# Kernel optimization log

Hardware: AMD Instinct MI355X
Metric: run time of the kernel (lower is better)

The kernel has to match this reference:

```python
import jax, jax.numpy as jnp
import numpy as np

# dims (match init_kwargs)
B, S, HID = 2, 2048, 2048
NH = 16
DN = 128   # qk_nope_head_dim
DR = 64    # qk_rope_head_dim
DV = 128   # v_head_dim
QLR = 1536 # q_lora_rank
KVLR = 512 # kv_lora_rank
QHD = DN + DR  # 192
ROPE_BASE = 10000.0
EPS = 1e-6


def rms_norm(x, w):
    # ZeroCenteredRMSNorm: weight is zero-centered, scale = (1 + w)
    var = jnp.mean(x * x, axis=-1, keepdims=True)
    return x * jax.lax.rsqrt(var + EPS) * (1.0 + w)


def rotate_half(x):
    d = x.shape[-1] // 2
    return jnp.concatenate([-x[..., d:], x[..., :d]], axis=-1)


def deinterleave(x):
    # rearrange '(d_pairs two) -> (two d_pairs)'
    return jnp.concatenate([x[..., 0::2], x[..., 1::2]], axis=-1)


def setup_inputs() -> dict:
    key = jax.random.key(0)
    ks = jax.random.split(key, 8)
    s = 0.02
    return {
        "hidden_states": jax.random.normal(ks[0], (B, S, HID), jnp.float32),
        "position_ids": jnp.arange(S, dtype=jnp.int32),
        "Wq_down": jax.random.normal(ks[1], (HID, QLR), jnp.float32) * s,
        "q_norm_w": jnp.zeros((QLR,), jnp.float32),
        "Wq_up": jax.random.normal(ks[2], (QLR, NH * QHD), jnp.float32) * s,
        "Wkv_down": jax.random.normal(ks[3], (HID, KVLR + DR), jnp.float32) * s,
        "kv_norm_w": jnp.zeros((KVLR,), jnp.float32),
        "Wkv_up": jax.random.normal(ks[4], (KVLR, NH * (DN + DV)), jnp.float32) * s,
        "W_gate": jax.random.normal(ks[5], (HID, NH * DV), jnp.float32) * s,
        "W_out": jax.random.normal(ks[6], (NH * DV, HID), jnp.float32) * s,
    }


def reference(hidden_states, position_ids, Wq_down, q_norm_w, Wq_up,
              Wkv_down, kv_norm_w, Wkv_up, W_gate, W_out):
    bsz, q_len, _ = hidden_states.shape
    pos = jnp.broadcast_to(position_ids[None, :], (bsz, q_len))  # [b,s]

    # Q path: down-proj -> RMSNorm -> up-proj -> [b,h,s,QHD]
    q = rms_norm(hidden_states @ Wq_down, q_norm_w) @ Wq_up
    q = q.reshape(bsz, q_len, NH, QHD).transpose(0, 2, 1, 3)
    q_nope, q_rope = q[..., :DN], q[..., DN:]

    # KV path: joint down-proj -> split latent / rope key
    ckv = hidden_states @ Wkv_down                     # [b,s,KVLR+DR]
    c_kv, k_rope = ckv[..., :KVLR], ckv[..., KVLR:]
    k_rope = k_rope[:, None, :, :]                     # [b,1,s,DR]
    kv = rms_norm(c_kv, kv_norm_w) @ Wkv_up            # [b,s,NH*(DN+DV)]
    kv = kv.reshape(bsz, q_len, NH, DN + DV).transpose(0, 2, 1, 3)
    k_nope, v = kv[..., :DN], kv[..., DN:]

    # partial RoPE on rope dims (with the '(pairs two)->(two pairs)' permute)
    inv_freq = 1.0 / (ROPE_BASE ** (jnp.arange(0, DR, 2, dtype=jnp.float32) / DR))
    freqs = pos[..., None].astype(jnp.float32) * inv_freq  # [b,s,DR/2]
    emb = jnp.concatenate([freqs, freqs], axis=-1)          # [b,s,DR]
    cos = jnp.cos(emb)[:, None, :, :]                       # [b,1,s,DR]
    sin = jnp.sin(emb)[:, None, :, :]
    q_r = deinterleave(q_rope)
    k_r = deinterleave(k_rope)
    q_r = q_r * cos + rotate_half(q_r) * sin
    k_r = k_r * cos + rotate_half(k_r) * sin

    query = jnp.concatenate([q_nope, q_r], axis=-1)                       # [b,h,s,QHD]
    key = jnp.concatenate([k_nope, jnp.broadcast_to(k_r, k_nope.shape[:-1] + (DR,))], axis=-1)

    scores = jnp.einsum('bhqd,bhkd->bhqk', query, key) / np.sqrt(QHD)
    attn = jax.nn.softmax(scores, axis=-1)
    out = jnp.einsum('bhqk,bhkd->bhqd', attn, v)                          # [b,h,s,DV]
    out = out.transpose(0, 2, 1, 3)                                       # [b,s,h,DV]

    gate = jax.nn.sigmoid(hidden_states @ W_gate).reshape(bsz, q_len, NH, DV)
    out = (out * gate).reshape(bsz, q_len, NH * DV)
    return out @ W_out
```

## Files before the change

kernel.cpp:

```cpp
#include <hip/hip_runtime.h>
#include <math.h>

#define BT 2
#define SL 2048
#define HIDN 2048
#define NHEADS 16
#define DNOPE 128
#define DROPE 64
#define DVAL 128
#define QHEAD 192
#define QLRANK 1536
#define KVLRANK 512
#define TTOK (BT * SL)
#define FN 4224
#define FC_CKV 1536
#define FC_ROPE 2048
#define FC_GATE 2176

typedef unsigned short u16;
typedef u16 u16x4 __attribute__((ext_vector_type(4)));
typedef u16 u16x8 __attribute__((ext_vector_type(8)));
typedef short bf16x8 __attribute__((ext_vector_type(8)));
typedef float f32x4 __attribute__((ext_vector_type(4)));

__device__ __forceinline__ u16 f2b(float f) {
    union { float f; unsigned u; } v; v.f = f;
    unsigned r = v.u + 0x7FFFu + ((v.u >> 16) & 1u);
    return (u16)(r >> 16);
}
__device__ __forceinline__ float b2f(u16 h) {
    union { unsigned u; float f; } v; v.u = ((unsigned)h) << 16;
    return v.f;
}
__device__ __forceinline__ float fexp2(float x) {
    float r;
    asm("v_exp_f32 %0, %1" : "=v"(r) : "v"(x));
    return r;
}

__device__ __forceinline__ void gl2lds16(const u16* g, u16* l) {
    __builtin_amdgcn_global_load_lds((const __attribute__((address_space(1))) unsigned int*)g,
                                     (__attribute__((address_space(3))) unsigned int*)l, 16, 0, 0);
}

__device__ __forceinline__ void tcast_tile(const float* __restrict__ in, u16* __restrict__ out,
                                           int R, int C, int tx, int ty, int t) {
    __shared__ u16 tile[64][72];
    const int c0 = tx * 64, r0 = ty * 64;
    const int tr = t >> 4, tc4 = (t & 15) * 4;
#pragma unroll
    for (int i = 0; i < 4; ++i) {
        const int r = tr + i * 16;
        const float4 v = *(const float4*)&in[(size_t)(r0 + r) * C + c0 + tc4];
        u16x4 u;
        u.x = f2b(v.x); u.y = f2b(v.y); u.z = f2b(v.z); u.w = f2b(v.w);
        *(u16x4*)&tile[r][tc4] = u;
    }
    __syncthreads();
#pragma unroll
    for (int i = 0; i < 4; ++i) {
        const int rr = tr + i * 16;
        u16x4 u;
        u.x = tile[tc4 + 0][rr];
        u.y = tile[tc4 + 1][rr];
        u.z = tile[tc4 + 2][rr];
        u.w = tile[tc4 + 3][rr];
        *(u16x4*)&out[(size_t)(c0 + rr) * R + r0 + tc4] = u;
    }
}

__global__ __launch_bounds__(256) void precast_k(
    const float* __restrict__ Wq_down, const float* __restrict__ Wq_up,
    const float* __restrict__ Wkv_down, const float* __restrict__ Wkv_up,
    const float* __restrict__ W_gate, const float* __restrict__ W_out,
    const float* __restrict__ hs, u16* __restrict__ wqd_t, u16* __restrict__ wqu_t,
    u16* __restrict__ wkvd_t, u16* __restrict__ wkvu_t, u16* __restrict__ wg_t,
    u16* __restrict__ wo_t, u16* __restrict__ hs16) {
    const int tid = blockIdx.x;
    const int t = threadIdx.x;
    if (tid >= 4768) {
        int i = (tid - 4768) * 256 + t;
        for (; i < TTOK * HIDN / 4; i += 2048 * 256) {
            const float4 v = ((const float4*)hs)[i];
            u16x4 u;
            u.x = f2b(v.x); u.y = f2b(v.y); u.z = f2b(v.z); u.w = f2b(v.w);
            ((u16x4*)hs16)[i] = u;
        }
        return;
    }
    if (tid < 768) {
        tcast_tile(Wq_down, wqd_t, 2048, 1536, tid % 24, tid / 24, t);
    } else if (tid < 1920) {
        const int i = tid - 768;
        tcast_tile(Wq_up, wqu_t, 1536, 3072, i % 48, i / 48, t);
    } else if (tid < 2208) {
        const int i = tid - 1920;
        tcast_tile(Wkv_down, wkvd_t, 2048, 576, i % 9, i / 9, t);
    } else if (tid < 2720) {
        const int i = tid - 2208;
        tcast_tile(Wkv_up, wkvu_t, 512, 4096, i % 64, i / 64, t);
    } else if (tid < 3744) {
        const int i = tid - 2720;
        tcast_tile(W_gate, wg_t, 2048, 2048, i % 32, i / 32, t);
    } else {
        const int i = tid - 3744;
        tcast_tile(W_out, wo_t, 2048, 2048, i % 32, i / 32, t);
    }
}

template <int MODE>
__global__ __launch_bounds__(256) void gemm_bf16_k(const u16* __restrict__ A,
                                                   const u16* __restrict__ Bt,
                                                   void* __restrict__ Cv, u16* __restrict__ C2,
                                                   int M, int N, int K) {
    __shared__ u16 As[128 * 64];
    __shared__ u16 Bs[128 * 64];
    const int t = threadIdx.x;
    const int nx = gridDim.x;
    const int bid = blockIdx.x + nx * blockIdx.y;
    const int cpx = (nx * gridDim.y) >> 3;
    const int swz = (bid & 7) * cpx + (bid >> 3);
    const int bn = (swz % nx) * 128, bm = (swz / nx) * 128;
    const int w = t >> 6, lane = t & 63;
    const int wr = (w >> 1) * 64, wc = (w & 1) * 64;
    const int lr = lane & 15, lg = lane >> 4;

    const int srow = w * 32 + (lane >> 3);
    const int scol = ((lane & 7) ^ ((lane >> 3) & 7)) * 8;
    const u16* Ag = A + (size_t)(bm + srow) * K + scol;
    const u16* Bg = Bt + (size_t)(bn + srow) * K + scol;
    u16* Asl = As + w * 2048;
    u16* Bsl = Bs + w * 2048;

    f32x4 acc[4][4];
#pragma unroll
    for (int i = 0; i < 4; ++i)
#pragma unroll
        for (int j = 0; j < 4; ++j) acc[i][j] = 0.f;

    for (int k0 = 0; k0 < K; k0 += 64) {
        __syncthreads();
#pragma unroll
        for (int j = 0; j < 4; ++j) gl2lds16(Ag + (size_t)(j * 8) * K + k0, Asl + j * 512);
#pragma unroll
        for (int j = 0; j < 4; ++j) gl2lds16(Bg + (size_t)(j * 8) * K + k0, Bsl + j * 512);
        __syncthreads();
#pragma unroll
        for (int kk = 0; kk < 2; ++kk) {
            bf16x8 af[4], bfr[4];
#pragma unroll
            for (int mi = 0; mi < 4; ++mi) {
                const int row = wr + mi * 16 + lr;
                const int idx = (row * 64 + kk * 32 + lg * 8) ^ ((row & 7) << 3);
                af[mi] = *(const bf16x8*)&As[idx];
            }
#pragma unroll
            for (int ni = 0; ni < 4; ++ni) {
                const int row = wc + ni * 16 + lr;
                const int idx = (row * 64 + kk * 32 + lg * 8) ^ ((row & 7) << 3);
                bfr[ni] = *(const bf16x8*)&Bs[idx];
            }
#pragma unroll
            for (int mi = 0; mi < 4; ++mi)
#pragma unroll
                for (int ni = 0; ni < 4; ++ni)
                    acc[mi][ni] = __builtin_amdgcn_mfma_f32_16x16x32_bf16(af[mi], bfr[ni],
                                                                          acc[mi][ni], 0, 0, 0);
        }
    }
#pragma unroll
    for (int mi = 0; mi < 4; ++mi)
#pragma unroll
        for (int ni = 0; ni < 4; ++ni) {
            const int row0 = bm + wr + mi * 16 + lg * 4;
            const int col = bn + wc + ni * 16 + lr;
            if (MODE == 3) {
                const int h = col >> 8, cd = col & 255;
                if (cd < 128) {
#pragma unroll
                    for (int r = 0; r < 4; ++r)
                        ((u16*)Cv)[(size_t)(row0 + r) * 2048 + h * 128 + cd] =
                            f2b(acc[mi][ni][r]);
                } else {
                    u16x4 pk;
                    pk.x = f2b(acc[mi][ni][0]);
                    pk.y = f2b(acc[mi][ni][1]);
                    pk.z = f2b(acc[mi][ni][2]);
                    pk.w = f2b(acc[mi][ni][3]);
                    const int bb = row0 >> 11;
                    *(u16x4*)&C2[((size_t)((bb * 16 + h) * 128 + (cd - 128))) * SL +
                                 (row0 & (SL - 1))] = pk;
                }
            } else {
#pragma unroll
                for (int r = 0; r < 4; ++r) {
                    float v = acc[mi][ni][r];
                    if (MODE == 2 && col >= FC_GATE) v = 1.f / (1.f + __expf(-v));
                    if (MODE == 1)
                        ((float*)Cv)[(size_t)(row0 + r) * N + col] = v;
                    else
                        ((u16*)Cv)[(size_t)(row0 + r) * N + col] = f2b(v);
                }
            }
        }
}

__global__ __launch_bounds__(256) void rms2_k(const u16* __restrict__ fout,
                                              const float* __restrict__ qw,
                                              const float* __restrict__ kw, u16* __restrict__ qn,
                                              u16* __restrict__ kvn) {
    const int rid = blockIdx.x;
    const bool isq = rid < TTOK;
    const int row = isq ? rid : rid - TTOK;
    const int n = isq ? QLRANK : KVLRANK;
    const u16* x = fout + (size_t)row * FN + (isq ? 0 : FC_CKV);
    const float* w = isq ? qw : kw;
    u16* y = isq ? (qn + (size_t)row * QLRANK) : (kvn + (size_t)row * KVLRANK);
    const int t = threadIdx.x;
    float ss = 0.f;
    for (int d = t * 4; d < n; d += 1024) {
        const u16x4 u = *(const u16x4*)&x[d];
        const float a = b2f(u.x), b = b2f(u.y), c = b2f(u.z), e = b2f(u.w);
        ss += a * a + b * b + c * c + e * e;
    }
    ss += __shfl_down(ss, 32);
    ss += __shfl_down(ss, 16);
    ss += __shfl_down(ss, 8);
    ss += __shfl_down(ss, 4);
    ss += __shfl_down(ss, 2);
    ss += __shfl_down(ss, 1);
    __shared__ float red[5];
    if ((t & 63) == 0) red[t >> 6] = ss;
    __syncthreads();
    if (t == 0) red[4] = rsqrtf((red[0] + red[1] + red[2] + red[3]) / (float)n + 1e-6f);
    __syncthreads();
    const float sc = red[4];
    for (int d = t * 4; d < n; d += 1024) {
        const u16x4 u = *(const u16x4*)&x[d];
        const float4 wv = *(const float4*)&w[d];
        u16x4 o;
        o.x = f2b(b2f(u.x) * sc * (1.f + wv.x));
        o.y = f2b(b2f(u.y) * sc * (1.f + wv.y));
        o.z = f2b(b2f(u.z) * sc * (1.f + wv.z));
        o.w = f2b(b2f(u.w) * sc * (1.f + wv.w));
        *(u16x4*)&y[d] = o;
    }
}

__global__ __launch_bounds__(64) void rope_k(u16* __restrict__ q, const u16* __restrict__ fout,
                                             u16* __restrict__ kr, const int* __restrict__ pos_ids) {
    const int tok = blockIdx.x * 2 + (threadIdx.x >> 5);
    const int j = threadIdx.x & 31;
    const int s = tok & (SL - 1);
    const float pos = (float)pos_ids[s];
    const float inv = 1.f / powf(10000.f, (float)(2 * j) / 64.f);
    const float f = pos * inv;
    const float c = cosf(f), sn = sinf(f);
    const u16* kc = fout + (size_t)tok * FN + FC_ROPE;
    const unsigned kp = *(const unsigned*)&kc[2 * j];
    const float ke = b2f((u16)(kp & 0xffff)), ko = b2f((u16)(kp >> 16));
    kr[tok * 64 + j] = f2b(ke * c - ko * sn);
    kr[tok * 64 + 32 + j] = f2b(ko * c + ke * sn);
#pragma unroll
    for (int h = 0; h < NHEADS; ++h) {
        u16* qb = q + (size_t)tok * (NHEADS * QHEAD) + h * QHEAD + DNOPE;
        const unsigned qp = *(const unsigned*)&qb[2 * j];
        const float qe = b2f((u16)(qp & 0xffff)), qo = b2f((u16)(qp >> 16));
        qb[j] = f2b(qe * c - qo * sn);
        qb[32 + j] = f2b(qo * c + qe * sn);
    }
}

#define PSTR 76
__global__ __launch_bounds__(256, 2) void mla_attn_k(const u16* __restrict__ qbuf,
                                                     const u16* __restrict__ knope,
                                                     const u16* __restrict__ kr,
                                                     const u16* __restrict__ vT,
                                                     const u16* __restrict__ gateb,
                                                     u16* __restrict__ outg) {
    __shared__ u16 Ks[64 * 200];
    __shared__ u16 Vt[128 * 72];
    __shared__ u16 Ps[4 * 32 * PSTR];
    const int bh = blockIdx.x;
    const int b = bh >> 4, h = bh & 15;
    const int q0 = blockIdx.y * 128;
    const int t = threadIdx.x, w = t >> 6, lane = t & 63;
    const int lr = lane & 15, lg = lane >> 4;
    const float qs = 0.07216878364870322f * 1.4426950408889634f;
    const float THR = 8.f * 1.4426950408889634f;

    int kRow[6], kC8[6];
#pragma unroll
    for (int c = 0; c < 6; ++c) {
        const int i = t + c * 256;
        kRow[c] = i / 24;
        kC8[c] = (i % 24) * 8;
    }
    int vRow[4], vC8[4];
#pragma unroll
    for (int c = 0; c < 4; ++c) {
        const int i = t + c * 256;
        vRow[c] = i >> 3;
        vC8[c] = (i & 7) * 8;
    }

    bf16x8 aq[2][6];
#pragma unroll
    for (int mi = 0; mi < 2; ++mi) {
        const int qrow = b * SL + q0 + w * 32 + mi * 16 + lr;
#pragma unroll
        for (int ks = 0; ks < 6; ++ks) {
            const u16x8 raw = *(const u16x8*)&qbuf[(size_t)qrow * (NHEADS * QHEAD) + h * QHEAD +
                                                   ks * 32 + lg * 8];
            bf16x8 o;
#pragma unroll
            for (int j = 0; j < 8; ++j) o[j] = (short)f2b(b2f(raw[j]) * qs);
            aq[mi][ks] = o;
        }
    }
    bf16x8 ones;
#pragma unroll
    for (int j = 0; j < 8; ++j) ones[j] = (short)0x3F80;

    f32x4 O[2][8];
#pragma unroll
    for (int mi = 0; mi < 2; ++mi)
#pragma unroll
        for (int df = 0; df < 8; ++df) O[mi][df] = 0.f;
    f32x4 Ol[2];
    Ol[0] = 0.f;
    Ol[1] = 0.f;
    float m[2][4];
#pragma unroll
    for (int mi = 0; mi < 2; ++mi)
#pragma unroll
        for (int r = 0; r < 4; ++r) m[mi][r] = -INFINITY;

    u16x8 kreg[6], vreg[4];
#define ATTN_ISSUE_K(K0)                                                                     \
    {                                                                                        \
        _Pragma("unroll") for (int c = 0; c < 6; ++c) {                                      \
            const int tok = b * SL + (K0) + kRow[c];                                         \
            kreg[c] = (kC8[c] < 128)                                                         \
                          ? *(const u16x8*)&knope[(size_t)tok * 2048 + h * 128 + kC8[c]]     \
                          : *(const u16x8*)&kr[(size_t)tok * 64 + (kC8[c] - 128)];           \
        }                                                                                    \
    }
#define ATTN_ISSUE_V(K0)                                                                     \
    {                                                                                        \
        _Pragma("unroll") for (int c = 0; c < 4; ++c)                                        \
            vreg[c] = *(const u16x8*)&vT[(size_t)(bh * 128 + vRow[c]) * SL + (K0) + vC8[c]]; \
    }

    ATTN_ISSUE_K(0);
    ATTN_ISSUE_V(0);

    for (int it = 0; it < SL / 64; ++it) {
        __syncthreads();
#pragma unroll
        for (int c = 0; c < 6; ++c) *(u16x8*)&Ks[kRow[c] * 200 + kC8[c]] = kreg[c];
#pragma unroll
        for (int c = 0; c < 4; ++c) *(u16x8*)&Vt[vRow[c] * 72 + vC8[c]] = vreg[c];
        __syncthreads();
        const bool more = (it + 1) < SL / 64;
        const int kn = (it + 1) * 64;
        if (more) ATTN_ISSUE_K(kn);

        f32x4 s[2][4];
#pragma unroll
        for (int mi = 0; mi < 2; ++mi)
#pragma unroll
            for (int nf = 0; nf < 4; ++nf) s[mi][nf] = 0.f;
#pragma unroll
        for (int ks = 0; ks < 6; ++ks) {
#pragma unroll
            for (int nf = 0; nf < 4; ++nf) {
                const bf16x8 bk = *(const bf16x8*)&Ks[(nf * 16 + lr) * 200 + ks * 32 + lg * 8];
                s[0][nf] = __builtin_amdgcn_mfma_f32_16x16x32_bf16(aq[0][ks], bk, s[0][nf], 0, 0, 0);
                s[1][nf] = __builtin_amdgcn_mfma_f32_16x16x32_bf16(aq[1][ks], bk, s[1][nf], 0, 0, 0);
            }
        }

        float g = -INFINITY;
#pragma unroll
        for (int mi = 0; mi < 2; ++mi)
#pragma unroll
            for (int r = 0; r < 4; ++r) {
                const float lmax =
                    fmaxf(fmaxf(s[mi][0][r], s[mi][1][r]), fmaxf(s[mi][2][r], s[mi][3][r]));
                g = fmaxf(g, lmax - m[mi][r]);
            }
        g = fmaxf(g, __shfl_xor(g, 1));
        g = fmaxf(g, __shfl_xor(g, 2));
        g = fmaxf(g, __shfl_xor(g, 4));
        g = fmaxf(g, __shfl_xor(g, 8));
        g = fmaxf(g, __shfl_xor(g, 16));
        g = fmaxf(g, __shfl_xor(g, 32));
        if (!(g <= THR)) {
#pragma unroll
            for (int mi = 0; mi < 2; ++mi)
#pragma unroll
                for (int r = 0; r < 4; ++r) {
                    float lm =
                        fmaxf(fmaxf(s[mi][0][r], s[mi][1][r]), fmaxf(s[mi][2][r], s[mi][3][r]));
                    lm = fmaxf(lm, __shfl_xor(lm, 1));
                    lm = fmaxf(lm, __shfl_xor(lm, 2));
                    lm = fmaxf(lm, __shfl_xor(lm, 4));
                    lm = fmaxf(lm, __shfl_xor(lm, 8));
                    const float mn = fmaxf(m[mi][r], lm);
                    const float al = fexp2(m[mi][r] - mn);
                    m[mi][r] = mn;
                    Ol[mi][r] *= al;
#pragma unroll
                    for (int df = 0; df < 8; ++df) O[mi][df][r] *= al;
                }
        }

#pragma unroll
        for (int mi = 0; mi < 2; ++mi) {
            const int pb = w * 32 * PSTR + mi * 16 * PSTR;
#pragma unroll
            for (int r = 0; r < 4; ++r) {
                const float mn = m[mi][r];
                const int prow = pb + (lg * 4 + r) * PSTR + lr;
                Ps[prow] = f2b(fexp2(s[mi][0][r] - mn));
                Ps[prow + 16] = f2b(fexp2(s[mi][1][r] - mn));
                Ps[prow + 32] = f2b(fexp2(s[mi][2][r] - mn));
                Ps[prow + 48] = f2b(fexp2(s[mi][3][r] - mn));
            }
        }

        if (more) ATTN_ISSUE_V(kn);

        bf16x8 pa[2][2];
#pragma unroll
        for (int mi = 0; mi < 2; ++mi)
#pragma unroll
            for (int ks2 = 0; ks2 < 2; ++ks2)
                pa[mi][ks2] =
                    *(const bf16x8*)&Ps[w * 32 * PSTR + (mi * 16 + lr) * PSTR + ks2 * 32 + lg * 8];
#pragma unroll
        for (int mi = 0; mi < 2; ++mi)
#pragma unroll
            for (int ks2 = 0; ks2 < 2; ++ks2)
                Ol[mi] = __builtin_amdgcn_mfma_f32_16x16x32_bf16(pa[mi][ks2], ones, Ol[mi], 0, 0, 0);
#pragma unroll
        for (int df = 0; df < 8; ++df)
#pragma unroll
            for (int ks2 = 0; ks2 < 2; ++ks2) {
                const bf16x8 bv = *(const bf16x8*)&Vt[(df * 16 + lr) * 72 + ks2 * 32 + lg * 8];
                O[0][df] = __builtin_amdgcn_mfma_f32_16x16x32_bf16(pa[0][ks2], bv, O[0][df], 0, 0, 0);
                O[1][df] = __builtin_amdgcn_mfma_f32_16x16x32_bf16(pa[1][ks2], bv, O[1][df], 0, 0, 0);
            }
    }
#pragma unroll
    for (int mi = 0; mi < 2; ++mi) {
        float invl[4];
#pragma unroll
        for (int r = 0; r < 4; ++r) invl[r] = 1.f / Ol[mi][r];
#pragma unroll
        for (int df = 0; df < 8; ++df)
#pragma unroll
            for (int r = 0; r < 4; ++r) {
                const int qq = b * SL + q0 + w * 32 + mi * 16 + lg * 4 + r;
                const int col = h * DVAL + df * 16 + lr;
                const float o = O[mi][df][r] * invl[r];
                const float gg = b2f(gateb[(size_t)qq * FN + col]);
                outg[(size_t)qq * (NHEADS * DVAL) + col] = f2b(o * gg);
            }
    }
}

extern "C" void kernel_launch(void* const* d_in, const int* in_sizes, int n_in, void* d_out,
                              int out_size, void* d_ws, size_t ws_size, hipStream_t stream) {
    const float* hs = (const float*)d_in[0];
    const int* pos = (const int*)d_in[1];
    const float* Wq_down = (const float*)d_in[2];
    const float* q_norm_w = (const float*)d_in[3];
    const float* Wq_up = (const float*)d_in[4];
    const float* Wkv_down = (const float*)d_in[5];
    const float* kv_norm_w = (const float*)d_in[6];
    const float* Wkv_up = (const float*)d_in[7];
    const float* W_gate = (const float*)d_in[8];
    const float* W_out = (const float*)d_in[9];
    float* out = (float*)d_out;

    u16* p = (u16*)d_ws;
    u16* hs16 = p;      p += (size_t)TTOK * HIDN;
    u16* wdown_t = p;   p += (size_t)FN * HIDN;
    u16* wqd_t = wdown_t;
    u16* wkvd_t = wdown_t + (size_t)QLRANK * HIDN;
    u16* wg_t = wdown_t + (size_t)FC_GATE * HIDN;
    u16* wqu_t = p;     p += (size_t)(NHEADS * QHEAD) * QLRANK;
    u16* wkvu_t = p;    p += (size_t)(NHEADS * 256) * KVLRANK;
    u16* wo_t = p;      p += (size_t)HIDN * (NHEADS * DVAL);
    u16* fout = p;      p += (size_t)TTOK * FN;
    u16* qdownN = p;    p += (size_t)TTOK * QLRANK;
    u16* qbuf = p;      p += (size_t)TTOK * (NHEADS * QHEAD);
    u16* kvn = p;       p += (size_t)TTOK * KVLRANK;
    u16* knope = p;     p += (size_t)TTOK * (NHEADS * DNOPE);
    u16* krb = p;       p += (size_t)TTOK * DROPE;
    u16* vTg = p;       p += (size_t)32 * 128 * SL;
    u16* outg = p;      p += (size_t)TTOK * (NHEADS * DVAL);

    const dim3 blk(256);

    precast_k<<<dim3(6816), blk, 0, stream>>>(Wq_down, Wq_up, Wkv_down, Wkv_up, W_gate, W_out, hs,
                                              wqd_t, wqu_t, wkvd_t, wkvu_t, wg_t, wo_t, hs16);

    gemm_bf16_k<2><<<dim3(FN / 128, TTOK / 128), blk, 0, stream>>>(hs16, wdown_t, fout, nullptr,
                                                                   TTOK, FN, HIDN);
    rms2_k<<<dim3(2 * TTOK), blk, 0, stream>>>(fout, q_norm_w, kv_norm_w, qdownN, kvn);
    gemm_bf16_k<0><<<dim3((NHEADS * QHEAD) / 128, TTOK / 128), blk, 0, stream>>>(
        qdownN, wqu_t, qbuf, nullptr, TTOK, NHEADS * QHEAD, QLRANK);
    gemm_bf16_k<3><<<dim3((NHEADS * 256) / 128, TTOK / 128), blk, 0, stream>>>(
        kvn, wkvu_t, knope, vTg, TTOK, NHEADS * 256, KVLRANK);
    rope_k<<<dim3(TTOK / 2), dim3(64), 0, stream>>>(qbuf, fout, krb, pos);

    mla_attn_k<<<dim3(32, SL / 128), blk, 0, stream>>>(qbuf, knope, krb, vTg, fout + FC_GATE, outg);

    gemm_bf16_k<1><<<dim3(HIDN / 128, TTOK / 128), blk, 0, stream>>>(outg, wo_t, out, nullptr, TTOK,
                                                                     HIDN, NHEADS * DVAL);
}
```

Baseline: 440.4 us.

## Merge Q and KV up-projection GEMMs into one launch; add MFMA wave priority in attention

```diff
diff --git a/kernel.cpp b/kernel.cpp
--- a/kernel.cpp
+++ b/kernel.cpp
@@ -111,8 +111,7 @@
 template <int MODE>
 __global__ __launch_bounds__(256) void gemm_bf16_k(const u16* __restrict__ A,
                                                    const u16* __restrict__ Bt,
-                                                   void* __restrict__ Cv, u16* __restrict__ C2,
-                                                   int M, int N, int K) {
+                                                   void* __restrict__ Cv, int M, int N, int K) {
     __shared__ u16 As[128 * 64];
     __shared__ u16 Bs[128 * 64];
     const int t = threadIdx.x;
@@ -174,13 +173,101 @@
         for (int ni = 0; ni < 4; ++ni) {
             const int row0 = bm + wr + mi * 16 + lg * 4;
             const int col = bn + wc + ni * 16 + lr;
-            if (MODE == 3) {
+#pragma unroll
+            for (int r = 0; r < 4; ++r) {
+                float v = acc[mi][ni][r];
+                if (MODE == 2 && col >= FC_GATE) v = 1.f / (1.f + __expf(-v));
+                if (MODE == 1)
+                    ((float*)Cv)[(size_t)(row0 + r) * N + col] = v;
+                else
+                    ((u16*)Cv)[(size_t)(row0 + r) * N + col] = f2b(v);
+            }
+        }
+}
+
+__global__ __launch_bounds__(256) void gemm_up_k(const u16* __restrict__ Aq,
+                                                 const u16* __restrict__ Akv,
+                                                 const u16* __restrict__ Btq,
+                                                 const u16* __restrict__ Btkv,
+                                                 u16* __restrict__ qbuf, u16* __restrict__ knope,
+                                                 u16* __restrict__ vT) {
+    __shared__ u16 As[128 * 64];
+    __shared__ u16 Bs[128 * 64];
+    const int t = threadIdx.x;
+    const int nx = gridDim.x;
+    const int bid = blockIdx.x + nx * blockIdx.y;
+    const int cpx = (nx * gridDim.y) >> 3;
+    const int swz = (bid & 7) * cpx + (bid >> 3);
+    const int tn = swz % nx, bm = (swz / nx) * 128;
+    const bool isq = tn < 24;
+    const int K = isq ? QLRANK : KVLRANK;
+    const int bn = (isq ? tn : tn - 24) * 128;
+    const u16* A = isq ? Aq : Akv;
+    const u16* Bt = isq ? Btq : Btkv;
+
+    const int w = t >> 6, lane = t & 63;
+    const int wr = (w >> 1) * 64, wc = (w & 1) * 64;
+    const int lr = lane & 15, lg = lane >> 4;
+
+    const int srow = w * 32 + (lane >> 3);
+    const int scol = ((lane & 7) ^ ((lane >> 3) & 7)) * 8;
+    const u16* Ag = A + (size_t)(bm + srow) * K + scol;
+    const u16* Bg = Bt + (size_t)(bn + srow) * K + scol;
+    u16* Asl = As + w * 2048;
+    u16* Bsl = Bs + w * 2048;
+
+    f32x4 acc[4][4];
+#pragma unroll
+    for (int i = 0; i < 4; ++i)
+#pragma unroll
+        for (int j = 0; j < 4; ++j) acc[i][j] = 0.f;
+
+    for (int k0 = 0; k0 < K; k0 += 64) {
+        __syncthreads();
+#pragma unroll
+        for (int j = 0; j < 4; ++j) gl2lds16(Ag + (size_t)(j * 8) * K + k0, Asl + j * 512);
+#pragma unroll
+        for (int j = 0; j < 4; ++j) gl2lds16(Bg + (size_t)(j * 8) * K + k0, Bsl + j * 512);
+        __syncthreads();
+#pragma unroll
+        for (int kk = 0; kk < 2; ++kk) {
+            bf16x8 af[4], bfr[4];
+#pragma unroll
+            for (int mi = 0; mi < 4; ++mi) {
+                const int row = wr + mi * 16 + lr;
+                const int idx = (row * 64 + kk * 32 + lg * 8) ^ ((row & 7) << 3);
+                af[mi] = *(const bf16x8*)&As[idx];
+            }
+#pragma unroll
+            for (int ni = 0; ni < 4; ++ni) {
+                const int row = wc + ni * 16 + lr;
+                const int idx = (row * 64 + kk * 32 + lg * 8) ^ ((row & 7) << 3);
+                bfr[ni] = *(const bf16x8*)&Bs[idx];
+            }
+#pragma unroll
+            for (int mi = 0; mi < 4; ++mi)
+#pragma unroll
+                for (int ni = 0; ni < 4; ++ni)
+                    acc[mi][ni] = __builtin_amdgcn_mfma_f32_16x16x32_bf16(af[mi], bfr[ni],
+                                                                          acc[mi][ni], 0, 0, 0);
+        }
+    }
+#pragma unroll
+    for (int mi = 0; mi < 4; ++mi)
+#pragma unroll
+        for (int ni = 0; ni < 4; ++ni) {
+            const int row0 = bm + wr + mi * 16 + lg * 4;
+            const int col = bn + wc + ni * 16 + lr;
+            if (isq) {
+#pragma unroll
+                for (int r = 0; r < 4; ++r)
+                    qbuf[(size_t)(row0 + r) * (NHEADS * QHEAD) + col] = f2b(acc[mi][ni][r]);
+            } else {
                 const int h = col >> 8, cd = col & 255;
                 if (cd < 128) {
 #pragma unroll
                     for (int r = 0; r < 4; ++r)
-                        ((u16*)Cv)[(size_t)(row0 + r) * 2048 + h * 128 + cd] =
-                            f2b(acc[mi][ni][r]);
+                        knope[(size_t)(row0 + r) * 2048 + h * 128 + cd] = f2b(acc[mi][ni][r]);
                 } else {
                     u16x4 pk;
                     pk.x = f2b(acc[mi][ni][0]);
@@ -188,18 +275,8 @@
                     pk.z = f2b(acc[mi][ni][2]);
                     pk.w = f2b(acc[mi][ni][3]);
                     const int bb = row0 >> 11;
-                    *(u16x4*)&C2[((size_t)((bb * 16 + h) * 128 + (cd - 128))) * SL +
+                    *(u16x4*)&vT[((size_t)((bb * 16 + h) * 128 + (cd - 128))) * SL +
                                  (row0 & (SL - 1))] = pk;
-                }
-            } else {
-#pragma unroll
-                for (int r = 0; r < 4; ++r) {
-                    float v = acc[mi][ni][r];
-                    if (MODE == 2 && col >= FC_GATE) v = 1.f / (1.f + __expf(-v));
-                    if (MODE == 1)
-                        ((float*)Cv)[(size_t)(row0 + r) * N + col] = v;
-                    else
-                        ((u16*)Cv)[(size_t)(row0 + r) * N + col] = f2b(v);
                 }
             }
         }
@@ -371,6 +448,7 @@
         for (int mi = 0; mi < 2; ++mi)
 #pragma unroll
             for (int nf = 0; nf < 4; ++nf) s[mi][nf] = 0.f;
+        __builtin_amdgcn_s_setprio(1);
 #pragma unroll
         for (int ks = 0; ks < 6; ++ks) {
 #pragma unroll
@@ -380,6 +458,7 @@
                 s[1][nf] = __builtin_amdgcn_mfma_f32_16x16x32_bf16(aq[1][ks], bk, s[1][nf], 0, 0, 0);
             }
         }
+        __builtin_amdgcn_s_setprio(0);
 
         float g = -INFINITY;
 #pragma unroll
@@ -439,6 +518,7 @@
             for (int ks2 = 0; ks2 < 2; ++ks2)
                 pa[mi][ks2] =
                     *(const bf16x8*)&Ps[w * 32 * PSTR + (mi * 16 + lr) * PSTR + ks2 * 32 + lg * 8];
+        __builtin_amdgcn_s_setprio(1);
 #pragma unroll
         for (int mi = 0; mi < 2; ++mi)
 #pragma unroll
@@ -452,6 +532,7 @@
                 O[0][df] = __builtin_amdgcn_mfma_f32_16x16x32_bf16(pa[0][ks2], bv, O[0][df], 0, 0, 0);
                 O[1][df] = __builtin_amdgcn_mfma_f32_16x16x32_bf16(pa[1][ks2], bv, O[1][df], 0, 0, 0);
             }
+        __builtin_amdgcn_s_setprio(0);
     }
 #pragma unroll
     for (int mi = 0; mi < 2; ++mi) {
@@ -508,17 +589,15 @@
     precast_k<<<dim3(6816), blk, 0, stream>>>(Wq_down, Wq_up, Wkv_down, Wkv_up, W_gate, W_out, hs,
                                               wqd_t, wqu_t, wkvd_t, wkvu_t, wg_t, wo_t, hs16);
 
-    gemm_bf16_k<2><<<dim3(FN / 128, TTOK / 128), blk, 0, stream>>>(hs16, wdown_t, fout, nullptr,
-                                                                   TTOK, FN, HIDN);
+    gemm_bf16_k<2><<<dim3(FN / 128, TTOK / 128), blk, 0, stream>>>(hs16, wdown_t, fout, TTOK, FN,
+                                                                   HIDN);
     rms2_k<<<dim3(2 * TTOK), blk, 0, stream>>>(fout, q_norm_w, kv_norm_w, qdownN, kvn);
-    gemm_bf16_k<0><<<dim3((NHEADS * QHEAD) / 128, TTOK / 128), blk, 0, stream>>>(
-        qdownN, wqu_t, qbuf, nullptr, TTOK, NHEADS * QHEAD, QLRANK);
-    gemm_bf16_k<3><<<dim3((NHEADS * 256) / 128, TTOK / 128), blk, 0, stream>>>(
-        kvn, wkvu_t, knope, vTg, TTOK, NHEADS * 256, KVLRANK);
+    gemm_up_k<<<dim3(56, TTOK / 128), blk, 0, stream>>>(qdownN, kvn, wqu_t, wkvu_t, qbuf, knope,
+                                                        vTg);
     rope_k<<<dim3(TTOK / 2), dim3(64), 0, stream>>>(qbuf, fout, krb, pos);
 
     mla_attn_k<<<dim3(32, SL / 128), blk, 0, stream>>>(qbuf, knope, krb, vTg, fout + FC_GATE, outg);
 
-    gemm_bf16_k<1><<<dim3(HIDN / 128, TTOK / 128), blk, 0, stream>>>(outg, wo_t, out, nullptr, TTOK,
-                                                                     HIDN, NHEADS * DVAL);
-}
+    gemm_bf16_k<1><<<dim3(HIDN / 128, TTOK / 128), blk, 0, stream>>>(outg, wo_t, out, TTOK, HIDN,
+                                                                     NHEADS * DVAL);
+}
```

Measured after the change: 452.6 us. 2.8% more time.
